# Optimization experiments

Measured on AMD Instinct MI355X. Metric: run time of the kernel, lower is better.

The kernel has to match this reference:

```python
import jax, jax.numpy as jnp
import numpy as np

N_HEADS, D_MODEL, D_HEAD = 16, 1024, 64
INIT_STD = 0.02
IGNORE = -100000.0


def setup_inputs() -> dict:
    key = jax.random.key(0)
    ks = jax.random.split(key, 5)
    x = jax.random.normal(ks[0], (2, 2048, D_MODEL), dtype=jnp.float32)
    W_Q = INIT_STD * jax.random.normal(ks[1], (N_HEADS, D_MODEL, D_HEAD), dtype=jnp.float32)
    W_K = INIT_STD * jax.random.normal(ks[2], (N_HEADS, D_MODEL, D_HEAD), dtype=jnp.float32)
    W_V = INIT_STD * jax.random.normal(ks[3], (N_HEADS, D_MODEL, D_HEAD), dtype=jnp.float32)
    W_O = INIT_STD * jax.random.normal(ks[4], (N_HEADS, D_HEAD, D_MODEL), dtype=jnp.float32)
    b_Q = jnp.zeros((N_HEADS, D_HEAD), dtype=jnp.float32)
    b_K = jnp.zeros((N_HEADS, D_HEAD), dtype=jnp.float32)
    b_V = jnp.zeros((N_HEADS, D_HEAD), dtype=jnp.float32)
    b_O = jnp.zeros((D_MODEL,), dtype=jnp.float32)
    return {"normalized_resid_pre": x, "W_Q": W_Q, "W_K": W_K, "W_V": W_V,
            "W_O": W_O, "b_Q": b_Q, "b_K": b_K, "b_V": b_V, "b_O": b_O}


def reference(normalized_resid_pre, W_Q, W_K, W_V, W_O, b_Q, b_K, b_V, b_O):
    x = normalized_resid_pre  # [b, s, d_model]
    q = jnp.einsum('bsm,hmd->bshd', x, W_Q) + b_Q  # [b, s, h, d_head]
    k = jnp.einsum('bsm,hmd->bshd', x, W_K) + b_K
    v = jnp.einsum('bsm,hmd->bshd', x, W_V) + b_V
    scores = jnp.einsum('bqhd,bkhd->bhqk', q, k) / jnp.sqrt(jnp.float32(D_HEAD))
    s = x.shape[1]
    causal = jnp.triu(jnp.ones((s, s), dtype=bool), k=1)  # True above diagonal
    scores = jnp.where(causal, jnp.float32(IGNORE), scores)
    pattern = jax.nn.softmax(scores, axis=-1)  # [b, h, q, k]
    z = jnp.einsum('bkhd,bhqk->bqhd', v, pattern)
    attn_out = jnp.einsum('bqhd,hdm->bqm', z, W_O) + b_O
    return attn_out
```

## Files before the change

### kernel.cpp

```cpp
#include <hip/hip_runtime.h>
#include <hip/hip_bf16.h>

#define BB   2
#define SS   2048
#define HH   16
#define DM_  1024
#define DH_  64
#define NROW 4096
#define NQKV 3072

typedef unsigned short u16;
typedef unsigned int u32;
using short4v = __attribute__((ext_vector_type(4))) short;
using short8 = __attribute__((ext_vector_type(8))) short;
using bf16x8 = __attribute__((ext_vector_type(8))) __bf16;
using f32x4  = __attribute__((ext_vector_type(4))) float;
using f32x16 = __attribute__((ext_vector_type(16))) float;

#define QSCALE 0.180336880f

__device__ __forceinline__ u16 f2bf(float f) {
    union { float f; unsigned u; } v; v.f = f;
    unsigned r = v.u + 0x7fffu + ((v.u >> 16) & 1u);
    return (u16)(r >> 16);
}

__device__ __forceinline__ f32x4 mfma16(bf16x8 a, bf16x8 b, f32x4 c) {
    return __builtin_amdgcn_mfma_f32_16x16x32_bf16(a, b, c, 0, 0, 0);
}
__device__ __forceinline__ f32x16 mfma32(bf16x8 a, bf16x8 b, f32x16 c) {
    return __builtin_amdgcn_mfma_f32_32x32x16_bf16(a, b, c, 0, 0, 0);
}

__device__ __forceinline__ u32 cvtpk(float lo, float hi) {
    u32 r;
    asm("v_cvt_pk_bf16_f32 %0, %1, %2" : "=v"(r) : "v"(lo), "v"(hi));
    return r;
}
#define PLSWAP(a, b) asm("v_permlane32_swap_b32 %0, %1" : "+v"(a), "+v"(b))

__device__ __forceinline__ float fexp2(float x) {
#if __has_builtin(__builtin_amdgcn_exp2f)
    return __builtin_amdgcn_exp2f(x);
#else
    float r; asm("v_exp_f32 %0, %1" : "=v"(r) : "v"(x)); return r;
#endif
}

__device__ __forceinline__ void gload16(const void* g, void* l) {
    __builtin_amdgcn_global_load_lds(
        (const __attribute__((address_space(1))) void*)g,
        (__attribute__((address_space(3))) void*)l, 16, 0, 0);
}

__device__ const int SCHED_QT[25]   = {15,15,14,14,13,13,12,6,12,11,11,10,5,10,9,9,8,4,8,7,7,3,2,1,0};
__device__ const int SCHED_HALF[25] = { 0, 1, 0, 1, 0, 1, 0,2, 1, 0, 1, 0,2, 1,0,1,0,2,1,0,1,2,2,2,2};

__global__ __launch_bounds__(256)
void prep(const float* __restrict__ x,  const float* __restrict__ wq,
          const float* __restrict__ wk, const float* __restrict__ wv,
          const float* __restrict__ wo, const float* __restrict__ bq,
          const float* __restrict__ bk, const float* __restrict__ bv,
          u16* __restrict__ Xb, u16* __restrict__ Wt,
          u16* __restrict__ WoT, float* __restrict__ biasQKV) {
    __shared__ float tile[64][65];
    const int bx = blockIdx.x, t = threadIdx.x;
    if (bx < 512) {
        const int tid = bx * 256 + t;
        #pragma unroll
        for (int it = 0; it < 8; ++it) {
            int i = tid + it * 131072;
            float4 v = ((const float4*)x)[i];
            u16 b4[4] = {f2bf(v.x), f2bf(v.y), f2bf(v.z), f2bf(v.w)};
            ((short4v*)Xb)[i] = *(short4v*)b4;
        }
        if (tid < NQKV) {
            int mat = tid >> 10, h = (tid >> 6) & 15, d = tid & 63;
            const float* bb = (mat == 0) ? bq : ((mat == 1) ? bk : bv);
            biasQKV[tid] = bb[h * DH_ + d];
        }
    } else if (bx < 1280) {
        const int idx = bx - 512;
        const int m0 = (idx & 15) * 64, hm = idx >> 4;
        const int mat = hm >> 4, h = hm & 15;
        const float* w = (mat == 0) ? wq : ((mat == 1) ? wk : wv);
        #pragma unroll
        for (int it = 0; it < 4; ++it) {
            int row = it * 16 + (t >> 4), c4 = (t & 15) * 4;
            float4 v = *(const float4*)&w[((size_t)h * 1024 + m0 + row) * 64 + c4];
            tile[row][c4] = v.x; tile[row][c4 + 1] = v.y;
            tile[row][c4 + 2] = v.z; tile[row][c4 + 3] = v.w;
        }
        __syncthreads();
        #pragma unroll
        for (int it = 0; it < 2; ++it) {
            int c = it * 256 + t, d = c >> 3, mc = (c & 7) * 8;
            u16 buf[8];
            #pragma unroll
            for (int j = 0; j < 8; ++j) buf[j] = f2bf(tile[mc + j][d]);
            *(short8*)&Wt[((size_t)(mat * 1024 + h * 64 + d)) * 1024 + m0 + mc] = *(short8*)buf;
        }
    } else {
        const int idx = bx - 1280;
        const int n0 = (idx & 15) * 64, k0 = (idx >> 4) * 64;
        #pragma unroll
        for (int it = 0; it < 4; ++it) {
            int row = it * 16 + (t >> 4), c4 = (t & 15) * 4;
            float4 v = *(const float4*)&wo[(size_t)(k0 + row) * DM_ + n0 + c4];
            tile[row][c4] = v.x; tile[row][c4 + 1] = v.y;
            tile[row][c4 + 2] = v.z; tile[row][c4 + 3] = v.w;
        }
        __syncthreads();
        #pragma unroll
        for (int it = 0; it < 2; ++it) {
            int c = it * 256 + t, n = c >> 3, kc = (c & 7) * 8;
            u16 buf[8];
            #pragma unroll
            for (int j = 0; j < 8; ++j) buf[j] = f2bf(tile[kc + j][n]);
            *(short8*)&WoT[(size_t)(n0 + n) * DM_ + k0 + kc] = *(short8*)buf;
        }
    }
}

__device__ __forceinline__ void gemm_core_128(
    const u16* __restrict__ Ap, const u16* __restrict__ Bp,
    int brow, int bcol, u16* lds, f32x4 acc[4][2]) {
    const int t = threadIdx.x, l = t & 63;
    const int wid = t >> 6, wm = wid >> 2, wn = wid & 3;
    const int c0 = t, c1 = t + 512;
    const int r0 = c0 >> 3, sb0 = ((c0 & 7) ^ (r0 & 7)) << 3;
    const int r1 = c1 >> 3, sb1 = ((c1 & 7) ^ (r1 & 7)) << 3;
    u16* A0 = lds;
    u16* B0 = lds + 16384;
    const int rA0 = wm * 64 + (l & 15);
    const int rB0 = wn * 32 + (l & 15);
    const int sw  = (l & 7) << 3;
    const int colA = ((l >> 4) << 3);

    {
        gload16(Ap + (size_t)(brow + r0) * DM_ + sb0, A0 + c0 * 8);
        gload16(Ap + (size_t)(brow + r1) * DM_ + sb1, A0 + c1 * 8);
        gload16(Bp + (size_t)(bcol + r0) * DM_ + sb0, B0 + c0 * 8);
        gload16(Bp + (size_t)(bcol + r1) * DM_ + sb1, B0 + c1 * 8);
    }
    __syncthreads();
    for (int kt = 0; kt < 16; ++kt) {
        const int p = kt & 1;
        if (kt < 15) {
            const int ko = (kt + 1) * 64;
            gload16(Ap + (size_t)(brow + r0) * DM_ + ko + sb0, A0 + (p ^ 1) * 8192 + c0 * 8);
            gload16(Ap + (size_t)(brow + r1) * DM_ + ko + sb1, A0 + (p ^ 1) * 8192 + c1 * 8);
            gload16(Bp + (size_t)(bcol + r0) * DM_ + ko + sb0, B0 + (p ^ 1) * 8192 + c0 * 8);
            gload16(Bp + (size_t)(bcol + r1) * DM_ + ko + sb1, B0 + (p ^ 1) * 8192 + c1 * 8);
        }
        const u16* Ab = A0 + p * 8192;
        const u16* Bb = B0 + p * 8192;
        #pragma unroll
        for (int kc = 0; kc < 64; kc += 32) {
            const int cx = (kc + colA) ^ sw;
            bf16x8 af[4], bfr[2];
            #pragma unroll
            for (int m = 0; m < 4; ++m)
                af[m] = *(const bf16x8*)(Ab + (rA0 + m * 16) * 64 + cx);
            #pragma unroll
            for (int n = 0; n < 2; ++n)
                bfr[n] = *(const bf16x8*)(Bb + (rB0 + n * 16) * 64 + cx);
            __builtin_amdgcn_s_setprio(1);
            #pragma unroll
            for (int m = 0; m < 4; ++m)
                #pragma unroll
                for (int n = 0; n < 2; ++n)
                    acc[m][n] = mfma16(af[m], bfr[n], acc[m][n]);
            __builtin_amdgcn_s_setprio(0);
        }
        __syncthreads();
    }
}

__global__ __launch_bounds__(512)
void gemm_qkv3(const u16* __restrict__ Xb, const u16* __restrict__ Wt,
               const float* __restrict__ bias, u16* __restrict__ Qs,
               u16* __restrict__ Ks, u16* __restrict__ Vt) {
    __shared__ __align__(16) u16 lds[32768];
    const int bx = blockIdx.x, t = threadIdx.x, l = t & 63;
    const int wid = t >> 6, wm = wid >> 2, wn = wid & 3;
    f32x4 acc[4][2] = {};
    const bool isV = (bx >= 512);
    int brow, bcol; const u16 *Ap, *Bp;
    if (!isV) { brow = (bx & 31) * 128; bcol = (bx >> 5) * 128; Ap = Xb; Bp = Wt; }
    else { int i2 = bx - 512; brow = (i2 & 7) * 128; bcol = (i2 >> 3) * 128;
           Ap = Wt + (size_t)2048 * DM_; Bp = Xb; }
    gemm_core_128(Ap, Bp, brow, bcol, lds, acc);

    u16* wr_ = lds + wid * 2048;
    const int colbase = bcol + wn * 32;
    const int rowbase = brow + wm * 64;
    const int rsub = ((l >> 4) << 2);
    if (!isV) {
        const float b0 = bias[colbase + (l & 15)];
        const float b1 = bias[colbase + 16 + (l & 15)];
        const float scl = (colbase < 1024) ? QSCALE : 1.0f;
        #pragma unroll
        for (int m = 0; m < 4; ++m)
            #pragma unroll
            for (int n = 0; n < 2; ++n) {
                const float bb = n ? b1 : b0;
                #pragma unroll
                for (int r = 0; r < 4; ++r)
                    wr_[(m * 16 + rsub + r) * 32 + n * 16 + (l & 15)] =
                        f2bf((acc[m][n][r] + bb) * scl);
            }
    } else {
        #pragma unroll
        for (int m = 0; m < 4; ++m) {
            float4 bv = *(const float4*)&bias[2048 + rowbase + m * 16 + rsub];
            const float bbr[4] = {bv.x, bv.y, bv.z, bv.w};
            #pragma unroll
            for (int n = 0; n < 2; ++n)
                #pragma unroll
                for (int r = 0; r < 4; ++r)
                    wr_[(m * 16 + rsub + r) * 32 + n * 16 + (l & 15)] =
                        f2bf(acc[m][n][r] + bbr[r]);
        }
    }
    __syncthreads();
    if (!isV) {
        const int hsel = (colbase >> 6) & 15, d0 = colbase & 63;
        const int bsel = rowbase >> 11, s0 = rowbase & 2047;
        u16* outp = (colbase < 1024) ? Qs : Ks;
        #pragma unroll
        for (int p = 0; p < 4; ++p) {
            const int rr = p * 16 + (l >> 2);
            short8 v = *(const short8*)(wr_ + rr * 32 + (l & 3) * 8);
            *(short8*)&outp[(((size_t)bsel * HH + hsel) * SS + s0 + rr) * DH_ + d0 + (l & 3) * 8] = v;
        }
    } else {
        const int bsel = colbase >> 11, s0 = colbase & 2047;
        #pragma unroll
        for (int p = 0; p < 4; ++p) {
            const int rr = p * 16 + (l >> 2);
            short8 v = *(const short8*)(wr_ + rr * 32 + (l & 3) * 8);
            *(short8*)&Vt[((size_t)bsel * 1024 + rowbase + rr) * SS + s0 + (l & 3) * 8] = v;
        }
    }
}

__global__ __launch_bounds__(512)
void gemm_out3(const u16* __restrict__ Zb, const u16* __restrict__ WoT,
               const float* __restrict__ bO, float* __restrict__ out) {
    __shared__ __align__(16) u16 lds[32768];
    const int bx = blockIdx.x, t = threadIdx.x, l = t & 63;
    const int wid = t >> 6, wm = wid >> 2, wn = wid & 3;
    const int brow = (bx & 31) * 128, bcol = (bx >> 5) * 128;
    f32x4 acc[4][2] = {};
    gemm_core_128(Zb, WoT, brow, bcol, lds, acc);
    const int colbase = bcol + wn * 32;
    const int rowbase = brow + wm * 64;
    const int rsub = ((l >> 4) << 2);
    const float b0 = bO[colbase + (l & 15)];
    const float b1 = bO[colbase + 16 + (l & 15)];
    #pragma unroll
    for (int m = 0; m < 4; ++m)
        #pragma unroll
        for (int n = 0; n < 2; ++n) {
            const float bb = n ? b1 : b0;
            #pragma unroll
            for (int r = 0; r < 4; ++r)
                out[(size_t)(rowbase + m * 16 + rsub + r) * DM_ + colbase + n * 16 + (l & 15)] =
                    acc[m][n][r] + bb;
        }
}

__global__ __launch_bounds__(512, 4)
void attn_fwd(const u16* __restrict__ Qs, const u16* __restrict__ Ks,
              const u16* __restrict__ Vt, u16* __restrict__ Zb,
              float* __restrict__ Po, float* __restrict__ Pl) {
    __shared__ __align__(16) u16 fK[2][8192];
    __shared__ __align__(16) u16 fV[2][8192];
    __shared__ float lrP[128];
    __shared__ float lrX[128];
    const int bidx = blockIdx.x;
    const int e  = bidx >> 5;
    const int bh = bidx & 31, b = bh >> 4, h = bh & 15;
    const int qt = SCHED_QT[e], half = SCHED_HALF[e];
    const bool issplit = (half < 2);
    const int nr = qt + 1;
    const int step = issplit ? 2 : 1;
    const int rfirst = issplit ? half : 0;
    const int cnt = issplit ? ((nr - half + 1) >> 1) : nr;
    const int t = threadIdx.x, wid = t >> 6, l = t & 63;
    const int hi = l >> 5, c32 = l & 31;
    const int qh = wid >> 1, par = wid & 1;
    const u16* Qp = Qs + (size_t)bh * SS * DH_;
    const u16* Kp = Ks + (size_t)bh * SS * DH_;
    const u16* Vp = Vt + (size_t)bh * DH_ * SS;
    const int qw = qt * 128 + qh * 32;

    bf16x8 aq[4];
    #pragma unroll
    for (int dk = 0; dk < 4; ++dk)
        aq[dk] = *(const bf16x8*)&Qp[(size_t)(qw + c32) * DH_ + dk * 16 + hi * 8];

    int kOff[2]; size_t vOff[2]; int dstc[2];
    #pragma unroll
    for (int i = 0; i < 2; ++i) {
        const int c = t + 512 * i, sec = c >> 6, ln = c & 63;
        const int kh = sec >> 3, s7 = sec & 7;
        kOff[i] = (kh * 64 + (s7 >> 2) * 32 + (ln & 31)) * DH_ + (s7 & 3) * 16 + (ln >> 5) * 8;
        vOff[i] = (size_t)((s7 >> 2) * 32 + (ln & 31)) * SS + kh * 64 + (s7 & 3) * 16 + (ln >> 5) * 8;
        dstc[i] = c * 8;
    }

    #define ISSUE(rr, pb)                                                     \
    {   const int ka = (rr) * 128;                                            \
        gload16(Kp + (size_t)ka * DH_ + kOff[0], &fK[pb][dstc[0]]);           \
        gload16(Kp + (size_t)ka * DH_ + kOff[1], &fK[pb][dstc[1]]);           \
        gload16(Vp + ka + vOff[0], &fV[pb][dstc[0]]);                         \
        gload16(Vp + ka + vOff[1], &fV[pb][dstc[1]]);                         \
    }

    ISSUE(rfirst, 0)
    __syncthreads();

    f32x16 o0 = {}, o1 = {};
    float lrp[4] = {0.f, 0.f, 0.f, 0.f};

    int r = rfirst;
    for (int i = 0; i < cnt; ++i, r += step) {
        const int p = i & 1;
        if (i + 1 < cnt) ISSUE(r + step, p ^ 1)
        const int kv0 = r * 128 + par * 64;
        if (kv0 <= qw + 31) {
            const u16* fKb = &fK[p][par * 4096];
            const u16* fVb = &fV[p][par * 4096];
            const bool have1 = (kv0 + 32 <= qw + 31);
            f32x16 s0 = {}, s1 = {};
            __builtin_amdgcn_s_setprio(1);
            #pragma unroll
            for (int dk = 0; dk < 4; ++dk)
                s0 = mfma32(*(const bf16x8*)(fKb + dk * 512 + l * 8), aq[dk], s0);
            if (have1) {
                #pragma unroll
                for (int dk = 0; dk < 4; ++dk)
                    s1 = mfma32(*(const bf16x8*)(fKb + (4 + dk) * 512 + l * 8), aq[dk], s1);
            }
            __builtin_amdgcn_s_setprio(0);
            if (kv0 + 63 > qw) {
                const int q = qw + c32;
                #pragma unroll
                for (int r16 = 0; r16 < 16; ++r16) {
                    const int crow = (r16 & 3) + 8 * (r16 >> 2) + 4 * hi;
                    if (kv0 + crow > q) s0[r16] = -1e30f;
                }
                if (have1) {
                    #pragma unroll
                    for (int r16 = 0; r16 < 16; ++r16) {
                        const int crow = (r16 & 3) + 8 * (r16 >> 2) + 4 * hi;
                        if (kv0 + 32 + crow > q) s1[r16] = -1e30f;
                    }
                }
            }
            #pragma unroll
            for (int r16 = 0; r16 < 16; ++r16) {
                s0[r16] = fexp2(s0[r16]);
                lrp[r16 & 3] += s0[r16];
            }
            if (have1) {
                #pragma unroll
                for (int r16 = 0; r16 < 16; ++r16) {
                    s1[r16] = fexp2(s1[r16]);
                    lrp[r16 & 3] += s1[r16];
                }
            }
            __builtin_amdgcn_s_setprio(1);
            #define PV_STEP(PS, B8, KS)                                          \
            {                                                                    \
                u32 cA  = cvtpk(PS[B8 + 0], PS[B8 + 1]);                         \
                u32 cA2 = cvtpk(PS[B8 + 2], PS[B8 + 3]);                         \
                u32 cB  = cvtpk(PS[B8 + 4], PS[B8 + 5]);                         \
                u32 cB2 = cvtpk(PS[B8 + 6], PS[B8 + 7]);                         \
                PLSWAP(cA, cB); PLSWAP(cA2, cB2);                                \
                u32 w[4] = {cA, cA2, cB, cB2};                                   \
                bf16x8 pa = *(bf16x8*)w;                                         \
                o0 = mfma32(pa, *(const bf16x8*)(fVb + (0 * 4 + (KS)) * 512 + l * 8), o0); \
                o1 = mfma32(pa, *(const bf16x8*)(fVb + (1 * 4 + (KS)) * 512 + l * 8), o1); \
            }
            PV_STEP(s0, 0, 0)
            PV_STEP(s0, 8, 1)
            if (have1) {
                PV_STEP(s1, 0, 2)
                PV_STEP(s1, 8, 3)
            }
            #undef PV_STEP
            __builtin_amdgcn_s_setprio(0);
        }
        __syncthreads();
    }
    #undef ISSUE

    float lrow = (lrp[0] + lrp[1]) + (lrp[2] + lrp[3]);
    lrow += __shfl_xor(lrow, 32);

    float* mrg = (float*)fK;
    __syncthreads();
    if (par) {
        #pragma unroll
        for (int e2 = 0; e2 < 16; ++e2) mrg[qh * 2048 + e2 * 64 + l] = o0[e2];
        #pragma unroll
        for (int e2 = 0; e2 < 16; ++e2) mrg[qh * 2048 + (16 + e2) * 64 + l] = o1[e2];
        if (hi == 0) lrP[qh * 32 + c32] = lrow;
    }
    __syncthreads();
    if (!par) {
        #pragma unroll
        for (int e2 = 0; e2 < 16; ++e2) o0[e2] += mrg[qh * 2048 + e2 * 64 + l];
        #pragma unroll
        for (int e2 = 0; e2 < 16; ++e2) o1[e2] += mrg[qh * 2048 + (16 + e2) * 64 + l];
        lrow += lrP[qh * 32 + c32];
        if (issplit) {
            float* po = Po + ((size_t)((bh * 9 + (qt - 7)) * 2 + half)) * 8192;
            #pragma unroll
            for (int r16 = 0; r16 < 16; ++r16) {
                const int lq = qh * 32 + (r16 & 3) + 8 * (r16 >> 2) + 4 * hi;
                po[lq * 64 + c32]      = o0[r16];
                po[lq * 64 + 32 + c32] = o1[r16];
            }
            if (hi == 0)
                Pl[((bh * 9 + (qt - 7)) * 2 + half) * 128 + qh * 32 + c32] = lrow;
        } else {
            lrX[qh * 32 + c32] = lrow;
            float invv[16];
            #pragma unroll
            for (int g = 0; g < 4; ++g) {
                float4 lv = *(const float4*)&lrX[qh * 32 + 8 * g + 4 * hi];
                invv[g * 4 + 0] = 1.0f / lv.x;
                invv[g * 4 + 1] = 1.0f / lv.y;
                invv[g * 4 + 2] = 1.0f / lv.z;
                invv[g * 4 + 3] = 1.0f / lv.w;
            }
            #pragma unroll
            for (int r16 = 0; r16 < 16; ++r16) {
                const int q = qw + (r16 & 3) + 8 * (r16 >> 2) + 4 * hi;
                u16* zp = &Zb[(((size_t)b * SS + q) * HH + h) * DH_];
                zp[c32]      = f2bf(o0[r16] * invv[r16]);
                zp[32 + c32] = f2bf(o1[r16] * invv[r16]);
            }
        }
    }
}

__global__ __launch_bounds__(256)
void attn_merge(const float* __restrict__ Po, const float* __restrict__ Pl,
                u16* __restrict__ Zb) {
    const int gid = blockIdx.x * 256 + threadIdx.x;
    if (gid >= 32 * 9 * 128 * 16) return;
    const int row = gid >> 4, dc = (gid & 15) * 4;
    const int bhq = row >> 7, lq = row & 127;
    const int bh = bhq / 9, qti = bhq - bh * 9;
    const int qt = qti + 7;
    const size_t baseA = ((size_t)(bh * 9 + qti) * 2) * 8192 + (size_t)lq * 64 + dc;
    const float* A = Po + baseA;
    const float* B = A + 8192;
    const float lA = Pl[((bh * 9 + qti) * 2) * 128 + lq];
    const float lB = Pl[((bh * 9 + qti) * 2 + 1) * 128 + lq];
    const float inv = 1.0f / (lA + lB);
    const int b = bh >> 4, h = bh & 15;
    const int q = qt * 128 + lq;
    u16 o4[4];
    #pragma unroll
    for (int i = 0; i < 4; ++i) o4[i] = f2bf((A[i] + B[i]) * inv);
    *(short4v*)&Zb[(((size_t)b * SS + q) * HH + h) * DH_ + dc] = *(short4v*)o4;
}

extern "C" void kernel_launch(void* const* d_in, const int* in_sizes, int n_in,
                              void* d_out, int out_size, void* d_ws, size_t ws_size,
                              hipStream_t stream) {
    const float* x  = (const float*)d_in[0];
    const float* wq = (const float*)d_in[1];
    const float* wk = (const float*)d_in[2];
    const float* wv = (const float*)d_in[3];
    const float* wo = (const float*)d_in[4];
    const float* bq = (const float*)d_in[5];
    const float* bk = (const float*)d_in[6];
    const float* bv = (const float*)d_in[7];
    const float* bO = (const float*)d_in[8];
    float* out = (float*)d_out;

    char* w = (char*)d_ws;
    u16* Xb  = (u16*)w;  w += (size_t)NROW * DM_ * 2;
    u16* Wt  = (u16*)w;  w += (size_t)NQKV * DM_ * 2;
    u16* WoT = (u16*)w;  w += (size_t)DM_ * DM_ * 2;
    float* biasQKV = (float*)w; w += (size_t)NQKV * 4;
    u16* Qs  = (u16*)w;  w += (size_t)BB * HH * SS * DH_ * 2;
    u16* Ks  = (u16*)w;  w += (size_t)BB * HH * SS * DH_ * 2;
    u16* Vt  = (u16*)w;  w += (size_t)BB * HH * SS * DH_ * 2;
    u16* Zb  = (u16*)w;  w += (size_t)BB * HH * SS * DH_ * 2;
    float* Po = (float*)w; w += (size_t)32 * 9 * 2 * 128 * 64 * 4;
    float* Pl = (float*)w; w += (size_t)32 * 9 * 2 * 128 * 4;

    prep<<<1536, 256, 0, stream>>>(x, wq, wk, wv, wo, bq, bk, bv,
                                   Xb, Wt, WoT, biasQKV);
    gemm_qkv3<<<768, 512, 0, stream>>>(Xb, Wt, biasQKV, Qs, Ks, Vt);
    attn_fwd<<<800, 512, 0, stream>>>(Qs, Ks, Vt, Zb, Po, Pl);
    attn_merge<<<2304, 256, 0, stream>>>(Po, Pl, Zb);
    gemm_out3<<<256, 512, 0, stream>>>(Zb, WoT, bO, out);
}
```

Measured before the change: 96.48 us.

## Retile output GEMM to 64x128 double-buffered blocks and store split partials in bf16

The output projection GEMM now uses 256-thread blocks with 64x128 tiles, 512 blocks instead of 256, and an explicit LDS double buffer that prefetches the next K slice while the current one is multiplied. The aim is more concurrent blocks across the CUs and load latency hidden behind MFMA work. The split-attention partial outputs are also written and read as bf16 instead of fp32, which halves partial-buffer traffic between attn_fwd and attn_merge. The cost is some precision in the unnormalized partial sums before merging.

```diff
diff --git a/kernel.cpp b/kernel.cpp
--- a/kernel.cpp
+++ b/kernel.cpp
@@ -23,6 +23,9 @@
     union { float f; unsigned u; } v; v.f = f;
     unsigned r = v.u + 0x7fffu + ((v.u >> 16) & 1u);
     return (u16)(r >> 16);
+}
+__device__ __forceinline__ float bf2f(u16 b) {
+    union { unsigned u; float f; } v; v.u = ((unsigned)b) << 16; return v.f;
 }
 
 __device__ __forceinline__ f32x4 mfma16(bf16x8 a, bf16x8 b, f32x4 c) {
@@ -245,36 +248,87 @@
     }
 }
 
-__global__ __launch_bounds__(512)
-void gemm_out3(const u16* __restrict__ Zb, const u16* __restrict__ WoT,
+__global__ __launch_bounds__(256)
+void gemm_out4(const u16* __restrict__ Zb, const u16* __restrict__ WoT,
                const float* __restrict__ bO, float* __restrict__ out) {
-    __shared__ __align__(16) u16 lds[32768];
+    __shared__ __align__(16) u16 lds[2][12288];
     const int bx = blockIdx.x, t = threadIdx.x, l = t & 63;
-    const int wid = t >> 6, wm = wid >> 2, wn = wid & 3;
-    const int brow = (bx & 31) * 128, bcol = (bx >> 5) * 128;
-    f32x4 acc[4][2] = {};
-    gemm_core_128(Zb, WoT, brow, bcol, lds, acc);
-    const int colbase = bcol + wn * 32;
-    const int rowbase = brow + wm * 64;
+    const int wid = t >> 6, wm = wid >> 1, wn = wid & 1;
+    const int brow = (bx & 63) * 64, bcol = (bx >> 6) * 128;
+    const int rA[2]  = {t >> 3, (t + 256) >> 3};
+    const int sbA[2] = {(((t) & 7) ^ (rA[0] & 7)) << 3, (((t + 256) & 7) ^ (rA[1] & 7)) << 3};
+    int rB[4], sbB[4];
+    #pragma unroll
+    for (int i = 0; i < 4; ++i) {
+        const int c = t + 256 * i;
+        rB[i] = c >> 3; sbB[i] = ((c & 7) ^ (rB[i] & 7)) << 3;
+    }
+    const int rA0 = wm * 32 + (l & 15);
+    const int rB0 = wn * 64 + (l & 15);
+    const int sw  = (l & 7) << 3;
+    const int colA = ((l >> 4) << 3);
+    f32x4 acc[2][4] = {};
+
+    #pragma unroll
+    for (int i = 0; i < 2; ++i)
+        gload16(Zb + (size_t)(brow + rA[i]) * DM_ + sbA[i], &lds[0][(t + 256 * i) * 8]);
+    #pragma unroll
+    for (int i = 0; i < 4; ++i)
+        gload16(WoT + (size_t)(bcol + rB[i]) * DM_ + sbB[i], &lds[0][4096 + (t + 256 * i) * 8]);
+    __syncthreads();
+    for (int kt = 0; kt < 16; ++kt) {
+        const int p = kt & 1;
+        if (kt < 15) {
+            const int ko = (kt + 1) * 64;
+            #pragma unroll
+            for (int i = 0; i < 2; ++i)
+                gload16(Zb + (size_t)(brow + rA[i]) * DM_ + ko + sbA[i],
+                        &lds[p ^ 1][(t + 256 * i) * 8]);
+            #pragma unroll
+            for (int i = 0; i < 4; ++i)
+                gload16(WoT + (size_t)(bcol + rB[i]) * DM_ + ko + sbB[i],
+                        &lds[p ^ 1][4096 + (t + 256 * i) * 8]);
+        }
+        const u16* Ab = &lds[p][0];
+        const u16* Bb = &lds[p][4096];
+        #pragma unroll
+        for (int kc = 0; kc < 64; kc += 32) {
+            const int cx = (kc + colA) ^ sw;
+            bf16x8 af[2], bfr[4];
+            #pragma unroll
+            for (int m = 0; m < 2; ++m)
+                af[m] = *(const bf16x8*)(Ab + (rA0 + m * 16) * 64 + cx);
+            #pragma unroll
+            for (int n = 0; n < 4; ++n)
+                bfr[n] = *(const bf16x8*)(Bb + (rB0 + n * 16) * 64 + cx);
+            __builtin_amdgcn_s_setprio(1);
+            #pragma unroll
+            for (int m = 0; m < 2; ++m)
+                #pragma unroll
+                for (int n = 0; n < 4; ++n)
+                    acc[m][n] = mfma16(af[m], bfr[n], acc[m][n]);
+            __builtin_amdgcn_s_setprio(0);
+        }
+        __syncthreads();
+    }
     const int rsub = ((l >> 4) << 2);
-    const float b0 = bO[colbase + (l & 15)];
-    const float b1 = bO[colbase + 16 + (l & 15)];
-    #pragma unroll
-    for (int m = 0; m < 4; ++m)
-        #pragma unroll
-        for (int n = 0; n < 2; ++n) {
-            const float bb = n ? b1 : b0;
+    float bb[4];
+    #pragma unroll
+    for (int n = 0; n < 4; ++n) bb[n] = bO[bcol + wn * 64 + n * 16 + (l & 15)];
+    #pragma unroll
+    for (int m = 0; m < 2; ++m)
+        #pragma unroll
+        for (int n = 0; n < 4; ++n)
             #pragma unroll
             for (int r = 0; r < 4; ++r)
-                out[(size_t)(rowbase + m * 16 + rsub + r) * DM_ + colbase + n * 16 + (l & 15)] =
-                    acc[m][n][r] + bb;
-        }
+                out[(size_t)(brow + wm * 32 + m * 16 + rsub + r) * DM_ +
+                    bcol + wn * 64 + n * 16 + (l & 15)] = acc[m][n][r] + bb[n];
 }
 
 __global__ __launch_bounds__(512, 4)
 void attn_fwd(const u16* __restrict__ Qs, const u16* __restrict__ Ks,
               const u16* __restrict__ Vt, u16* __restrict__ Zb,
-              float* __restrict__ Po, float* __restrict__ Pl) {
+              u16* __restrict__ Po, float* __restrict__ Pl) {
     __shared__ __align__(16) u16 fK[2][8192];
     __shared__ __align__(16) u16 fV[2][8192];
     __shared__ float lrP[128];
@@ -418,12 +472,12 @@
         for (int e2 = 0; e2 < 16; ++e2) o1[e2] += mrg[qh * 2048 + (16 + e2) * 64 + l];
         lrow += lrP[qh * 32 + c32];
         if (issplit) {
-            float* po = Po + ((size_t)((bh * 9 + (qt - 7)) * 2 + half)) * 8192;
+            u16* po = Po + ((size_t)((bh * 9 + (qt - 7)) * 2 + half)) * 8192;
             #pragma unroll
             for (int r16 = 0; r16 < 16; ++r16) {
                 const int lq = qh * 32 + (r16 & 3) + 8 * (r16 >> 2) + 4 * hi;
-                po[lq * 64 + c32]      = o0[r16];
-                po[lq * 64 + 32 + c32] = o1[r16];
+                po[lq * 64 + c32]      = f2bf(o0[r16]);
+                po[lq * 64 + 32 + c32] = f2bf(o1[r16]);
             }
             if (hi == 0)
                 Pl[((bh * 9 + (qt - 7)) * 2 + half) * 128 + qh * 32 + c32] = lrow;
@@ -450,7 +504,7 @@
 }
 
 __global__ __launch_bounds__(256)
-void attn_merge(const float* __restrict__ Po, const float* __restrict__ Pl,
+void attn_merge(const u16* __restrict__ Po, const float* __restrict__ Pl,
                 u16* __restrict__ Zb) {
     const int gid = blockIdx.x * 256 + threadIdx.x;
     if (gid >= 32 * 9 * 128 * 16) return;
@@ -459,8 +513,8 @@
     const int bh = bhq / 9, qti = bhq - bh * 9;
     const int qt = qti + 7;
     const size_t baseA = ((size_t)(bh * 9 + qti) * 2) * 8192 + (size_t)lq * 64 + dc;
-    const float* A = Po + baseA;
-    const float* B = A + 8192;
+    short4v a4 = *(const short4v*)(Po + baseA);
+    short4v b4 = *(const short4v*)(Po + baseA + 8192);
     const float lA = Pl[((bh * 9 + qti) * 2) * 128 + lq];
     const float lB = Pl[((bh * 9 + qti) * 2 + 1) * 128 + lq];
     const float inv = 1.0f / (lA + lB);
@@ -468,7 +522,8 @@
     const int q = qt * 128 + lq;
     u16 o4[4];
     #pragma unroll
-    for (int i = 0; i < 4; ++i) o4[i] = f2bf((A[i] + B[i]) * inv);
+    for (int i = 0; i < 4; ++i)
+        o4[i] = f2bf((bf2f((u16)a4[i]) + bf2f((u16)b4[i])) * inv);
     *(short4v*)&Zb[(((size_t)b * SS + q) * HH + h) * DH_ + dc] = *(short4v*)o4;
 }
 
@@ -495,7 +550,7 @@
     u16* Ks  = (u16*)w;  w += (size_t)BB * HH * SS * DH_ * 2;
     u16* Vt  = (u16*)w;  w += (size_t)BB * HH * SS * DH_ * 2;
     u16* Zb  = (u16*)w;  w += (size_t)BB * HH * SS * DH_ * 2;
-    float* Po = (float*)w; w += (size_t)32 * 9 * 2 * 128 * 64 * 4;
+    u16* Po  = (u16*)w;  w += (size_t)32 * 9 * 2 * 128 * 64 * 2;
     float* Pl = (float*)w; w += (size_t)32 * 9 * 2 * 128 * 4;
 
     prep<<<1536, 256, 0, stream>>>(x, wq, wk, wv, wo, bq, bk, bv,
@@ -503,5 +558,5 @@
     gemm_qkv3<<<768, 512, 0, stream>>>(Xb, Wt, biasQKV, Qs, Ks, Vt);
     attn_fwd<<<800, 512, 0, stream>>>(Qs, Ks, Vt, Zb, Po, Pl);
     attn_merge<<<2304, 256, 0, stream>>>(Po, Pl, Zb);
-    gemm_out3<<<256, 512, 0, stream>>>(Zb, WoT, bO, out);
-}
+    gemm_out4<<<512, 256, 0, stream>>>(Zb, WoT, bO, out);
+}
```

Result: no change. 98.23 us (+1.8%).
